# Kernel tuning notes

Hardware: AMD Instinct MI355X
Metric: run time of the kernel (lower is better)

Reference implementation:

```python
import jax, jax.numpy as jnp
import numpy as np

HIDDEN = 300
INPUT_DIM = 300


def setup_inputs() -> dict:
    key = jax.random.key(0)
    k_in, k_wih, k_whh, k_bih, k_bhh = jax.random.split(key, 5)
    bound = 1.0 / np.sqrt(HIDDEN)  # PyTorch RNNCell init: U(-1/sqrt(H), 1/sqrt(H))
    inputs = jax.random.normal(k_in, (512, 512, INPUT_DIM), dtype=jnp.float32)
    W_ih = jax.random.uniform(k_wih, (HIDDEN, INPUT_DIM), jnp.float32, -bound, bound)
    W_hh = jax.random.uniform(k_whh, (HIDDEN, HIDDEN), jnp.float32, -bound, bound)
    b_ih = jax.random.uniform(k_bih, (HIDDEN,), jnp.float32, -bound, bound)
    b_hh = jax.random.uniform(k_bhh, (HIDDEN,), jnp.float32, -bound, bound)
    return {"inputs": inputs, "W_ih": W_ih, "W_hh": W_hh, "b_ih": b_ih, "b_hh": b_hh}


def reference(inputs, W_ih, W_hh, b_ih, b_hh):
    # inputs: [seq, batch, input_dim]; vanilla tanh RNNCell scanned over time.
    seq, bz, _ = inputs.shape
    # Precompute input projections for all timesteps in one big GEMM.
    x_proj = jnp.einsum('sbi,hi->sbh', inputs, W_ih) + b_ih + b_hh  # [seq, batch, H]

    def step(ht, xp):
        ht = jnp.tanh(xp + ht @ W_hh.T)
        return ht, None

    h0 = jnp.zeros((bz, HIDDEN), dtype=inputs.dtype)
    ht, _ = jax.lax.scan(step, h0, x_proj)
    return ht
```

## Files before the change

kernel.cpp:

```cpp
#include <hip/hip_runtime.h>


typedef unsigned short u16;
typedef unsigned int   u32;
typedef __attribute__((ext_vector_type(8)))  short bf16x8;
typedef __attribute__((ext_vector_type(4)))  float f32x4;
typedef __attribute__((ext_vector_type(16))) float f32x16;

#define HID 300
#define KP  320
#define SEQ 512
#define BZ  512
#define MTOT (SEQ*BZ)

__device__ __forceinline__ u16 f2bf(float f) {
    u32 u = __float_as_uint(f);
    return (u16)((u + 0x7FFFu + ((u >> 16) & 1u)) >> 16);
}
__device__ __forceinline__ float bf2f(u16 h) {
    return __uint_as_float((u32)h << 16);
}
__device__ __forceinline__ float tanh_fast(float x) {
    float e = __builtin_amdgcn_exp2f(x * 2.8853900817779268f);
    float r = __builtin_amdgcn_rcpf(e + 1.0f);
    return __builtin_fmaf(-2.0f, r, 1.0f);
}

__global__ void prep_kernel(const float* __restrict__ wih,
                            const float* __restrict__ whh,
                            const float* __restrict__ bih,
                            const float* __restrict__ bhh,
                            u16* __restrict__ wihp, u16* __restrict__ whhp,
                            float* __restrict__ bias) {
    int n = blockIdx.x, k = threadIdx.x;
    bool v = (n < HID) && (k < HID);
    int src = n * HID + k, dst = n * KP + k;
    wihp[dst] = v ? f2bf(wih[src]) : (u16)0;
    whhp[dst] = v ? f2bf(whh[src]) : (u16)0;
    if (k == 0) bias[n] = (n < HID) ? (bih[n] + bhh[n]) : 0.0f;
}

__global__ __launch_bounds__(512, 2) void xproj_kernel(
    const float* __restrict__ in, const u16* __restrict__ wihp,
    const float* __restrict__ bias, u16* __restrict__ xp) {
    __shared__ __align__(16) u16 As[128 * 20];
    __shared__ __align__(16) u16 Bs[320 * 40];

    const int tid = threadIdx.x;
    const int w = tid >> 6, l = tid & 63;
    const int l5 = l >> 5, l31 = l & 31;
    const int m0 = blockIdx.x * 128;
    const int mt = w & 3;
    const int par = w >> 2;

    f32x16 acc[5];
#pragma unroll
    for (int j = 0; j < 5; ++j)
#pragma unroll
        for (int r = 0; r < 16; ++r) acc[j][r] = 0.0f;

    const int ar = tid >> 2, aq = tid & 3;
    const int bn = tid >> 1, bc = tid & 1;

    f32x4 aP;
    bf16x8 bP0, bP1;
    {
        aP = *(const f32x4*)(in + (m0 + ar) * HID + aq * 4);
        bP0 = *(const bf16x8*)(wihp + bn * KP + bc * 8);
        if (tid < 128) bP1 = *(const bf16x8*)(wihp + (bn + 256) * KP + bc * 8);
    }

#pragma unroll 1
    for (int ks = 0; ks < 19; ++ks) {
        __syncthreads();
        {
            u32 w0 = (u32)f2bf(aP[0]) | ((u32)f2bf(aP[1]) << 16);
            u32 w1 = (u32)f2bf(aP[2]) | ((u32)f2bf(aP[3]) << 16);
            u32* p = (u32*)&As[ar * 20 + aq * 4];
            p[0] = w0; p[1] = w1;
        }
        *(bf16x8*)&Bs[bn * 40 + ((bc ^ (bn & 1)) * 8)] = bP0;
        if (tid < 128)
            *(bf16x8*)&Bs[(bn + 256) * 40 + ((bc ^ (bn & 1)) * 8)] = bP1;

        if (ks < 18) {
            int gk = (ks + 1) * 16 + aq * 4;
            if (gk < HID) {
                aP = *(const f32x4*)(in + (m0 + ar) * HID + gk);
            } else {
                aP[0] = aP[1] = aP[2] = aP[3] = 0.0f;
            }
            bP0 = *(const bf16x8*)(wihp + bn * KP + (ks + 1) * 16 + bc * 8);
            if (tid < 128)
                bP1 = *(const bf16x8*)(wihp + (bn + 256) * KP + (ks + 1) * 16 + bc * 8);
        }
        __syncthreads();

        bf16x8 a = *(const bf16x8*)&As[(mt * 32 + l31) * 20 + l5 * 8];
#pragma unroll
        for (int j = 0; j < 5; ++j) {
            int nt = 2 * j + par;
            bf16x8 b = *(const bf16x8*)&Bs[(nt * 32 + l31) * 40 + ((l5 ^ (l31 & 1)) * 8)];
            acc[j] = __builtin_amdgcn_mfma_f32_32x32x16_bf16(a, b, acc[j], 0, 0, 0);
        }
    }

#pragma unroll
    for (int j = 0; j < 5; ++j) {
        int nt = 2 * j + par;
        int n = nt * 32 + l31;
        if (n < HID) {
            float bs = bias[n];
#pragma unroll
            for (int reg = 0; reg < 16; ++reg) {
                int row = (reg & 3) + 8 * (reg >> 2) + 4 * l5;
                float v = acc[j][reg] + bs;
                xp[(m0 + mt * 32 + row) * HID + n] = f2bf(v);
            }
        }
    }
}

__global__ __launch_bounds__(512, 2) void rnn_recur_kernel(
    const u16* __restrict__ xp, const u16* __restrict__ whhp,
    float* __restrict__ out) {
    __shared__ __align__(16) u16 hbuf[16 * 328];

    const int tid = threadIdx.x;
    const int w = tid >> 6, l = tid & 63;
    const int b0 = blockIdx.x * 16;
    const int col = l & 15, kq = l >> 4;
    const bool has3 = (w < 4);
    const int nt0 = w, nt1 = w + 8, nt2 = w + 16;

    for (int i = tid; i < (16 * 328) / 2; i += 512) ((u32*)hbuf)[i] = 0;

    bf16x8 Bf0[10], Bf1[10], Bf2[10];
#pragma unroll
    for (int ks = 0; ks < 10; ++ks) {
        Bf0[ks] = *(const bf16x8*)(whhp + (nt0 * 16 + col) * KP + ks * 32 + kq * 8);
        Bf1[ks] = *(const bf16x8*)(whhp + (nt1 * 16 + col) * KP + ks * 32 + kq * 8);
        if (has3)
            Bf2[ks] = *(const bf16x8*)(whhp + (nt2 * 16 + col) * KP + ks * 32 + kq * 8);
    }

    int xoff[12], hoff[12];
#pragma unroll
    for (int i = 0; i < 3; ++i) {
        int nt = (i == 0) ? nt0 : ((i == 1) ? nt1 : nt2);
        int n = nt * 16 + col;
#pragma unroll
        for (int r = 0; r < 4; ++r) {
            xoff[i * 4 + r] = (n < HID) ? ((b0 + kq * 4 + r) * HID + n) : -1;
            hoff[i * 4 + r] = (n < KP) ? ((kq * 4 + r) * 328 + n) : -1;
        }
    }

    u16 xc[12];
#pragma unroll
    for (int q = 0; q < 12; ++q) {
        u16 v = 0;
        if (xoff[q] >= 0) v = xp[xoff[q]];
        xc[q] = v;
    }

    __syncthreads();

#pragma unroll 1
    for (int t = 0; t < SEQ; ++t) {
        const int tn = (t < SEQ - 1) ? (t + 1) : (SEQ - 1);
        const int tbase = tn * (BZ * HID);
        u16 xn[12];
#pragma unroll
        for (int q = 0; q < 12; ++q) {
            u16 v = 0;
            if (xoff[q] >= 0) v = xp[tbase + xoff[q]];
            xn[q] = v;
        }

        f32x4 a0, a1, a2;
#pragma unroll
        for (int r = 0; r < 4; ++r) { a0[r] = 0.f; a1[r] = 0.f; a2[r] = 0.f; }

#pragma unroll
        for (int ks = 0; ks < 10; ++ks) {
            bf16x8 av = *(const bf16x8*)&hbuf[col * 328 + ks * 32 + kq * 8];
            a0 = __builtin_amdgcn_mfma_f32_16x16x32_bf16(av, Bf0[ks], a0, 0, 0, 0);
            a1 = __builtin_amdgcn_mfma_f32_16x16x32_bf16(av, Bf1[ks], a1, 0, 0, 0);
            if (has3)
                a2 = __builtin_amdgcn_mfma_f32_16x16x32_bf16(av, Bf2[ks], a2, 0, 0, 0);
        }
        __syncthreads();

#pragma unroll
        for (int r = 0; r < 4; ++r) {
            float c0 = a0[r] + bf2f(xc[r]);
            if (hoff[r] >= 0) hbuf[hoff[r]] = f2bf(tanh_fast(c0));
            float c1 = a1[r] + bf2f(xc[4 + r]);
            if (hoff[4 + r] >= 0) hbuf[hoff[4 + r]] = f2bf(tanh_fast(c1));
            float c2 = a2[r] + bf2f(xc[8 + r]);
            if (hoff[8 + r] >= 0) hbuf[hoff[8 + r]] = f2bf(tanh_fast(c2));
        }
        __syncthreads();

#pragma unroll
        for (int q = 0; q < 12; ++q) xc[q] = xn[q];
    }

    for (int i = tid; i < 16 * HID; i += 512) {
        int row = i / HID, n = i - row * HID;
        out[(b0 + row) * HID + n] = bf2f(hbuf[row * 328 + n]);
    }
}

extern "C" void kernel_launch(void* const* d_in, const int* in_sizes, int n_in,
                              void* d_out, int out_size, void* d_ws, size_t ws_size,
                              hipStream_t stream) {
    const float* in  = (const float*)d_in[0];
    const float* wih = (const float*)d_in[1];
    const float* whh = (const float*)d_in[2];
    const float* bih = (const float*)d_in[3];
    const float* bhh = (const float*)d_in[4];

    char* ws = (char*)d_ws;
    const size_t XP_BYTES = (size_t)MTOT * HID * sizeof(u16);
    u16*   xpb  = (u16*)ws;
    u16*   wihp = (u16*)(ws + XP_BYTES);
    u16*   whhp = (u16*)(ws + XP_BYTES + (size_t)KP * KP * 2);
    float* bias = (float*)(ws + XP_BYTES + 2 * (size_t)KP * KP * 2);

    prep_kernel<<<KP, KP, 0, stream>>>(wih, whh, bih, bhh, wihp, whhp, bias);
    xproj_kernel<<<MTOT / 128, 512, 0, stream>>>(in, wihp, bias, xpb);
    rnn_recur_kernel<<<BZ / 16, 512, 0, stream>>>(xpb, whhp, (float*)d_out);
}
```

Before: 1.176 ms.

## Double-buffer xproj GEMM with direct-to-LDS loads and restructure recurrence with ping-pong state

The input-projection GEMM now uses K-steps of 32 with double-buffered LDS, and loads W_ih straight into LDS with global_load_lds while the next A tile is prefetched. The recurrence kernel drops to 256 threads with 5 output tiles per wave. It swaps the MFMA operand roles, ping-pongs the hidden state between two LDS buffers so one barrier per step is removed, and prefetches x two steps ahead with vector loads. This aims to cut barrier and load latency on the serial path, at the cost of larger register pressure from the 50 weight fragments held per thread.

```diff
diff --git a/kernel.cpp b/kernel.cpp
--- a/kernel.cpp
+++ b/kernel.cpp
@@ -4,8 +4,11 @@
 typedef unsigned short u16;
 typedef unsigned int   u32;
 typedef __attribute__((ext_vector_type(8)))  short bf16x8;
+typedef __attribute__((ext_vector_type(4)))  short s16x4;
 typedef __attribute__((ext_vector_type(4)))  float f32x4;
 typedef __attribute__((ext_vector_type(16))) float f32x16;
+typedef __attribute__((ext_vector_type(2)))  unsigned int u32x2;
+typedef __attribute__((ext_vector_type(4)))  unsigned int u32x4;
 
 #define HID 300
 #define KP  320
@@ -24,6 +27,9 @@
     float e = __builtin_amdgcn_exp2f(x * 2.8853900817779268f);
     float r = __builtin_amdgcn_rcpf(e + 1.0f);
     return __builtin_fmaf(-2.0f, r, 1.0f);
+}
+__device__ __forceinline__ u32 pack2(float a, float b) {
+    return (u32)f2bf(a) | ((u32)f2bf(b) << 16);
 }
 
 __global__ void prep_kernel(const float* __restrict__ wih,
@@ -43,15 +49,16 @@
 __global__ __launch_bounds__(512, 2) void xproj_kernel(
     const float* __restrict__ in, const u16* __restrict__ wihp,
     const float* __restrict__ bias, u16* __restrict__ xp) {
-    __shared__ __align__(16) u16 As[128 * 20];
-    __shared__ __align__(16) u16 Bs[320 * 40];
+    __shared__ __align__(16) u16 As[2][4096];
+    __shared__ __align__(16) u16 Bs[2][10240];
 
     const int tid = threadIdx.x;
     const int w = tid >> 6, l = tid & 63;
-    const int l5 = l >> 5, l31 = l & 31;
+    const int mi = w & 3, ni = w >> 2;
+    const int l31 = l & 31, l5 = l >> 5;
     const int m0 = blockIdx.x * 128;
-    const int mt = w & 3;
-    const int par = w >> 2;
+
+    const int sm = tid >> 2, skg = tid & 3;
 
     f32x16 acc[5];
 #pragma unroll
@@ -59,157 +66,169 @@
 #pragma unroll
         for (int r = 0; r < 16; ++r) acc[j][r] = 0.0f;
 
-    const int ar = tid >> 2, aq = tid & 3;
-    const int bn = tid >> 1, bc = tid & 1;
-
-    f32x4 aP;
-    bf16x8 bP0, bP1;
+    auto loadA = [&](int it, f32x4& v0, f32x4& v1) {
+        int gk = it * 32 + skg * 8;
+        const float* p = in + (size_t)(m0 + sm) * HID + gk;
+        if (gk <= 292) { v0 = *(const f32x4*)p; v1 = *(const f32x4*)(p + 4); }
+        else if (gk <= 296) { v0 = *(const f32x4*)p; v1 = f32x4{0.f,0.f,0.f,0.f}; }
+        else { v0 = f32x4{0.f,0.f,0.f,0.f}; v1 = f32x4{0.f,0.f,0.f,0.f}; }
+    };
+    auto writeA = [&](int buf, const f32x4& v0, const f32x4& v1) {
+        u32x4 pk;
+        pk[0] = pack2(v0[0], v0[1]); pk[1] = pack2(v0[2], v0[3]);
+        pk[2] = pack2(v1[0], v1[1]); pk[3] = pack2(v1[2], v1[3]);
+        *(u32x4*)&As[buf][(skg >> 1) * 2048 + sm * 16 + (skg & 1) * 8] = pk;
+    };
+    auto stageB = [&](int buf, int it) {
+#pragma unroll
+        for (int s = 0; s < 3; ++s) {
+            int i = w + 8 * s;
+            if (i < 20) {
+                int c = i & 3, ng = i >> 2;
+                int n = ng * 64 + l;
+                const u16* g = wihp + n * KP + it * 32 + c * 8;
+                u16* d = &Bs[buf][c * 2560 + ng * 512];
+                __builtin_amdgcn_global_load_lds(
+                    (const __attribute__((address_space(1))) void*)g,
+                    (__attribute__((address_space(3))) void*)d, 16, 0, 0);
+            }
+        }
+    };
+
     {
-        aP = *(const f32x4*)(in + (m0 + ar) * HID + aq * 4);
-        bP0 = *(const bf16x8*)(wihp + bn * KP + bc * 8);
-        if (tid < 128) bP1 = *(const bf16x8*)(wihp + (bn + 256) * KP + bc * 8);
-    }
+        f32x4 v0, v1;
+        loadA(0, v0, v1);
+        writeA(0, v0, v1);
+        stageB(0, 0);
+    }
+    __syncthreads();
 
 #pragma unroll 1
-    for (int ks = 0; ks < 19; ++ks) {
+    for (int it = 0; it < 10; ++it) {
+        const int cb = it & 1, nb = (it + 1) & 1;
+        f32x4 v0, v1;
+        if (it < 9) {
+            loadA(it + 1, v0, v1);
+            stageB(nb, it + 1);
+        }
+#pragma unroll
+        for (int s = 0; s < 2; ++s) {
+            bf16x8 a = *(const bf16x8*)&As[cb][s * 2048 + mi * 512 + l31 * 16 + l5 * 8];
+#pragma unroll
+            for (int j = 0; j < 5; ++j) {
+                bf16x8 b = *(const bf16x8*)&Bs[cb][(s * 2 + l5) * 2560 + ((ni * 5 + j) * 32 + l31) * 8];
+                acc[j] = __builtin_amdgcn_mfma_f32_32x32x16_bf16(a, b, acc[j], 0, 0, 0);
+            }
+        }
+        if (it < 9) writeA(nb, v0, v1);
         __syncthreads();
-        {
-            u32 w0 = (u32)f2bf(aP[0]) | ((u32)f2bf(aP[1]) << 16);
-            u32 w1 = (u32)f2bf(aP[2]) | ((u32)f2bf(aP[3]) << 16);
-            u32* p = (u32*)&As[ar * 20 + aq * 4];
-            p[0] = w0; p[1] = w1;
-        }
-        *(bf16x8*)&Bs[bn * 40 + ((bc ^ (bn & 1)) * 8)] = bP0;
-        if (tid < 128)
-            *(bf16x8*)&Bs[(bn + 256) * 40 + ((bc ^ (bn & 1)) * 8)] = bP1;
-
-        if (ks < 18) {
-            int gk = (ks + 1) * 16 + aq * 4;
-            if (gk < HID) {
-                aP = *(const f32x4*)(in + (m0 + ar) * HID + gk);
-            } else {
-                aP[0] = aP[1] = aP[2] = aP[3] = 0.0f;
-            }
-            bP0 = *(const bf16x8*)(wihp + bn * KP + (ks + 1) * 16 + bc * 8);
-            if (tid < 128)
-                bP1 = *(const bf16x8*)(wihp + (bn + 256) * KP + (ks + 1) * 16 + bc * 8);
-        }
-        __syncthreads();
-
-        bf16x8 a = *(const bf16x8*)&As[(mt * 32 + l31) * 20 + l5 * 8];
-#pragma unroll
-        for (int j = 0; j < 5; ++j) {
-            int nt = 2 * j + par;
-            bf16x8 b = *(const bf16x8*)&Bs[(nt * 32 + l31) * 40 + ((l5 ^ (l31 & 1)) * 8)];
-            acc[j] = __builtin_amdgcn_mfma_f32_32x32x16_bf16(a, b, acc[j], 0, 0, 0);
-        }
-    }
-
-#pragma unroll
-    for (int j = 0; j < 5; ++j) {
-        int nt = 2 * j + par;
-        int n = nt * 32 + l31;
+    }
+
+    const int mbase = m0 + mi * 32;
+#pragma unroll
+    for (int j = 0; j < 5; ++j) {
+        int n = (ni * 5 + j) * 32 + l31;
         if (n < HID) {
             float bs = bias[n];
 #pragma unroll
             for (int reg = 0; reg < 16; ++reg) {
                 int row = (reg & 3) + 8 * (reg >> 2) + 4 * l5;
-                float v = acc[j][reg] + bs;
-                xp[(m0 + mt * 32 + row) * HID + n] = f2bf(v);
+                xp[(size_t)(mbase + row) * HID + n] = f2bf(acc[j][reg] + bs);
             }
         }
     }
 }
 
-__global__ __launch_bounds__(512, 2) void rnn_recur_kernel(
+__global__ __launch_bounds__(256, 1) void rnn_recur_kernel(
     const u16* __restrict__ xp, const u16* __restrict__ whhp,
     float* __restrict__ out) {
-    __shared__ __align__(16) u16 hbuf[16 * 328];
+    __shared__ __align__(16) u16 hb[2][16 * 328];
 
     const int tid = threadIdx.x;
-    const int w = tid >> 6, l = tid & 63;
+    const int w = tid >> 6;
+    const int l = tid & 63;
+    const int br = l & 15;
+    const int q  = l >> 4;
     const int b0 = blockIdx.x * 16;
-    const int col = l & 15, kq = l >> 4;
-    const bool has3 = (w < 4);
-    const int nt0 = w, nt1 = w + 8, nt2 = w + 16;
-
-    for (int i = tid; i < (16 * 328) / 2; i += 512) ((u32*)hbuf)[i] = 0;
-
-    bf16x8 Bf0[10], Bf1[10], Bf2[10];
-#pragma unroll
-    for (int ks = 0; ks < 10; ++ks) {
-        Bf0[ks] = *(const bf16x8*)(whhp + (nt0 * 16 + col) * KP + ks * 32 + kq * 8);
-        Bf1[ks] = *(const bf16x8*)(whhp + (nt1 * 16 + col) * KP + ks * 32 + kq * 8);
-        if (has3)
-            Bf2[ks] = *(const bf16x8*)(whhp + (nt2 * 16 + col) * KP + ks * 32 + kq * 8);
-    }
-
-    int xoff[12], hoff[12];
-#pragma unroll
-    for (int i = 0; i < 3; ++i) {
-        int nt = (i == 0) ? nt0 : ((i == 1) ? nt1 : nt2);
-        int n = nt * 16 + col;
-#pragma unroll
-        for (int r = 0; r < 4; ++r) {
-            xoff[i * 4 + r] = (n < HID) ? ((b0 + kq * 4 + r) * HID + n) : -1;
-            hoff[i * 4 + r] = (n < KP) ? ((kq * 4 + r) * 328 + n) : -1;
-        }
-    }
-
-    u16 xc[12];
-#pragma unroll
-    for (int q = 0; q < 12; ++q) {
-        u16 v = 0;
-        if (xoff[q] >= 0) v = xp[xoff[q]];
-        xc[q] = v;
+
+    for (int i = tid; i < (2 * 16 * 328) / 2; i += 256) ((u32*)hb)[i] = 0;
+
+    bf16x8 Af[5][10];
+#pragma unroll
+    for (int j = 0; j < 5; ++j) {
+        const u16* wrow = whhp + (size_t)((w + 4 * j) * 16 + br) * KP;
+#pragma unroll
+        for (int ks = 0; ks < 10; ++ks)
+            Af[j][ks] = *(const bf16x8*)(wrow + ks * 32 + q * 8);
+    }
+
+    int xo[5];
+#pragma unroll
+    for (int j = 0; j < 5; ++j) {
+        int n0 = (w + 4 * j) * 16 + q * 4;
+        xo[j] = (n0 < HID) ? ((b0 + br) * HID + n0) : -1;
+    }
+
+    const s16x4 z4 = {0, 0, 0, 0};
+    s16x4 xc[5], xn[5];
+#pragma unroll
+    for (int j = 0; j < 5; ++j) {
+        xc[j] = (xo[j] >= 0) ? *(const s16x4*)(xp + xo[j]) : z4;
+        xn[j] = (xo[j] >= 0) ? *(const s16x4*)(xp + (size_t)BZ * HID + xo[j]) : z4;
     }
 
     __syncthreads();
 
 #pragma unroll 1
     for (int t = 0; t < SEQ; ++t) {
-        const int tn = (t < SEQ - 1) ? (t + 1) : (SEQ - 1);
-        const int tbase = tn * (BZ * HID);
-        u16 xn[12];
-#pragma unroll
-        for (int q = 0; q < 12; ++q) {
-            u16 v = 0;
-            if (xoff[q] >= 0) v = xp[tbase + xoff[q]];
-            xn[q] = v;
-        }
-
-        f32x4 a0, a1, a2;
-#pragma unroll
-        for (int r = 0; r < 4; ++r) { a0[r] = 0.f; a1[r] = 0.f; a2[r] = 0.f; }
+        const u16* hc = hb[t & 1];
+        u16*       hn = hb[(t + 1) & 1];
+
+        s16x4 xf[5];
+        {
+            int t2 = (t + 2 < SEQ) ? (t + 2) : (SEQ - 1);
+            const u16* base = xp + (size_t)t2 * (BZ * HID);
+#pragma unroll
+            for (int j = 0; j < 5; ++j)
+                xf[j] = (xo[j] >= 0) ? *(const s16x4*)(base + xo[j]) : z4;
+        }
+
+        f32x4 acc[5];
+#pragma unroll
+        for (int j = 0; j < 5; ++j)
+#pragma unroll
+            for (int r = 0; r < 4; ++r) acc[j][r] = 0.0f;
 
 #pragma unroll
         for (int ks = 0; ks < 10; ++ks) {
-            bf16x8 av = *(const bf16x8*)&hbuf[col * 328 + ks * 32 + kq * 8];
-            a0 = __builtin_amdgcn_mfma_f32_16x16x32_bf16(av, Bf0[ks], a0, 0, 0, 0);
-            a1 = __builtin_amdgcn_mfma_f32_16x16x32_bf16(av, Bf1[ks], a1, 0, 0, 0);
-            if (has3)
-                a2 = __builtin_amdgcn_mfma_f32_16x16x32_bf16(av, Bf2[ks], a2, 0, 0, 0);
+            bf16x8 bfr = *(const bf16x8*)&hc[br * 328 + ks * 32 + q * 8];
+#pragma unroll
+            for (int j = 0; j < 5; ++j)
+                acc[j] = __builtin_amdgcn_mfma_f32_16x16x32_bf16(Af[j][ks], bfr, acc[j], 0, 0, 0);
+        }
+
+#pragma unroll
+        for (int j = 0; j < 5; ++j) {
+            int n0 = (w + 4 * j) * 16 + q * 4;
+            float v0 = tanh_fast(acc[j][0] + bf2f((u16)xc[j][0]));
+            float v1 = tanh_fast(acc[j][1] + bf2f((u16)xc[j][1]));
+            float v2 = tanh_fast(acc[j][2] + bf2f((u16)xc[j][2]));
+            float v3 = tanh_fast(acc[j][3] + bf2f((u16)xc[j][3]));
+            u32x2 pk;
+            pk[0] = pack2(v0, v1);
+            pk[1] = pack2(v2, v3);
+            *(u32x2*)&hn[br * 328 + n0] = pk;
         }
         __syncthreads();
 
 #pragma unroll
-        for (int r = 0; r < 4; ++r) {
-            float c0 = a0[r] + bf2f(xc[r]);
-            if (hoff[r] >= 0) hbuf[hoff[r]] = f2bf(tanh_fast(c0));
-            float c1 = a1[r] + bf2f(xc[4 + r]);
-            if (hoff[4 + r] >= 0) hbuf[hoff[4 + r]] = f2bf(tanh_fast(c1));
-            float c2 = a2[r] + bf2f(xc[8 + r]);
-            if (hoff[8 + r] >= 0) hbuf[hoff[8 + r]] = f2bf(tanh_fast(c2));
-        }
-        __syncthreads();
-
-#pragma unroll
-        for (int q = 0; q < 12; ++q) xc[q] = xn[q];
-    }
-
-    for (int i = tid; i < 16 * HID; i += 512) {
-        int row = i / HID, n = i - row * HID;
-        out[(b0 + row) * HID + n] = bf2f(hbuf[row * 328 + n]);
+        for (int j = 0; j < 5; ++j) { xc[j] = xn[j]; xn[j] = xf[j]; }
+    }
+
+    const u16* hf = hb[0];
+    for (int i = tid; i < 16 * HID; i += 256) {
+        int r = i / HID, n = i - r * HID;
+        out[(size_t)(b0 + r) * HID + n] = bf2f(hf[r * 328 + n]);
     }
 }
 
@@ -231,5 +250,5 @@
 
     prep_kernel<<<KP, KP, 0, stream>>>(wih, whh, bih, bhh, wihp, whhp, bias);
     xproj_kernel<<<MTOT / 128, 512, 0, stream>>>(in, wihp, bias, xpb);
-    rnn_recur_kernel<<<BZ / 16, 512, 0, stream>>>(xpb, whhp, (float*)d_out);
-}
+    rnn_recur_kernel<<<BZ / 16, 256, 0, stream>>>(xpb, whhp, (float*)d_out);
+}
```

New measurement: 1.177 ms. Within noise of the previous version (+0.1%).
